# Performance work log

Hardware: AMD Instinct MI355X
Metric: run time of the kernel (lower is better)

## Reference

```python
import jax, jax.numpy as jnp
import numpy as np

N_NODES = 100000   # n_nodes
N_EDGES = 1600000  # n_nodes * avg_degree(16)
D_IN = 128
D_OUT = 128


def setup_inputs() -> dict:
    key = jax.random.key(0)
    k1, k2, k3, k4, k5 = jax.random.split(key, 5)
    h = jax.random.normal(k1, (N_NODES, D_IN), dtype=jnp.float32)
    edge_src = jax.random.randint(k2, (N_EDGES,), 0, N_NODES, dtype=jnp.int32)
    edge_dst = jax.random.randint(k3, (N_EDGES,), 0, N_NODES, dtype=jnp.int32)
    # Linear params, init per reset_parameters: U(-stdv, stdv), stdv = 1/sqrt(in_feats)
    stdv = 1.0 / np.sqrt(D_IN)
    W = jax.random.uniform(k4, (D_OUT, D_IN), dtype=jnp.float32, minval=-stdv, maxval=stdv)
    b = jax.random.uniform(k5, (D_OUT,), dtype=jnp.float32, minval=-stdv, maxval=stdv)
    return {"h": h, "edge_src": edge_src, "edge_dst": edge_dst, "W": W, "b": b}


def reference(h, edge_src, edge_dst, W, b):
    # update_all(copy_src('h'), sum) == neighbor-sum aggregation (SpMM with 0/1 adjacency)
    ah = jax.ops.segment_sum(h[edge_src], edge_dst, num_segments=N_NODES)  # [N, D_IN]
    # dense linear + activation fused on the aggregated features
    return jax.nn.relu(ah @ W.T + b)  # [N, D_OUT]
```

## Files before the change

### kernel.cpp

```cpp
#include <hip/hip_runtime.h>

#define D 128
#define BKT_SHIFT 9
#define BKT_SIZE 512
#define P1_EPB 4096
#define CNT_BLOCKS 512
#define PARTIALS_INTS (512 * 256)
#define SORT_CAP 9216
#define SW_LDU 68

typedef __attribute__((ext_vector_type(8))) short bf16x8;
typedef __attribute__((ext_vector_type(4))) float f32x4;

__device__ inline unsigned int pack2bf(float a, float b) {
    unsigned int ua = __float_as_uint(a);
    unsigned int ub = __float_as_uint(b);
    ua = (ua + 0x7fffu + ((ua >> 16) & 1u)) >> 16;
    ub = (ub + 0x7fffu + ((ub >> 16) & 1u)) >> 16;
    return ua | (ub << 16);
}
__device__ inline unsigned short pack1bf(float a) {
    unsigned int ua = __float_as_uint(a);
    return (unsigned short)((ua + 0x7fffu + ((ua >> 16) & 1u)) >> 16);
}


__global__ __launch_bounds__(256) void bucket_count_kernel(
    const int* __restrict__ edst, int* __restrict__ partials, int n_edges, int epb)
{
    __shared__ int hcnt[256];
    const int tid = threadIdx.x;
    hcnt[tid] = 0;
    __syncthreads();
    const int base = blockIdx.x * epb;
    const int lim = min(epb, n_edges - base);
    int k = tid;
    for (; k + 768 < lim; k += 1024) {
        int d0 = edst[base + k];
        int d1 = edst[base + k + 256];
        int d2 = edst[base + k + 512];
        int d3 = edst[base + k + 768];
        atomicAdd(&hcnt[d0 >> BKT_SHIFT], 1);
        atomicAdd(&hcnt[d1 >> BKT_SHIFT], 1);
        atomicAdd(&hcnt[d2 >> BKT_SHIFT], 1);
        atomicAdd(&hcnt[d3 >> BKT_SHIFT], 1);
    }
    for (; k < lim; k += 256)
        atomicAdd(&hcnt[edst[base + k] >> BKT_SHIFT], 1);
    __syncthreads();
    partials[(blockIdx.x << 8) + tid] = hcnt[tid];
}

__global__ __launch_bounds__(256) void bucket_scan_kernel(
    const int* __restrict__ partials, int* __restrict__ bucketBase,
    int* __restrict__ bucketCur, int nbk)
{
    __shared__ int s[256];
    const int t = threadIdx.x;
    int sum = 0;
    #pragma unroll 8
    for (int b = 0; b < CNT_BLOCKS; b++) sum += partials[(b << 8) + t];
    int v = (t < nbk) ? sum : 0;
    s[t] = v;
    __syncthreads();
    #pragma unroll
    for (int off = 1; off < 256; off <<= 1) {
        int x = (t >= off) ? s[t - off] : 0;
        __syncthreads();
        s[t] += x;
        __syncthreads();
    }
    if (t < nbk) {
        int base = s[t] - v;
        bucketBase[t] = base;
        bucketCur[t] = base;
    }
}

__global__ __launch_bounds__(256) void p1_partition_kernel(
    const int* __restrict__ esrc, const int* __restrict__ edst,
    int* __restrict__ bucketCur, unsigned int* __restrict__ pairs, int n_edges)
{
    __shared__ int hist[256];
    __shared__ int lbase[256];
    __shared__ int gbase[256];
    __shared__ int cur[256];
    __shared__ unsigned int buf[P1_EPB];
    __shared__ unsigned char bkt8[P1_EPB];
    const int tid = threadIdx.x;
    const int base = blockIdx.x * P1_EPB;
    hist[tid] = 0;
    __syncthreads();
    unsigned int pk[16]; int bk[16];
    #pragma unroll
    for (int k = 0; k < 16; k++) {
        int e = base + k * 256 + tid;
        if (e < n_edges) {
            int sv = esrc[e], dv = edst[e];
            bk[k] = dv >> BKT_SHIFT;
            pk[k] = ((unsigned)sv << BKT_SHIFT) | (unsigned)(dv & (BKT_SIZE - 1));
            atomicAdd(&hist[bk[k]], 1);
        } else bk[k] = -1;
    }
    __syncthreads();
    const int v = hist[tid];
    if (v > 0) gbase[tid] = atomicAdd(&bucketCur[tid], v);
    lbase[tid] = v;
    __syncthreads();
    #pragma unroll
    for (int off = 1; off < 256; off <<= 1) {
        int x = (tid >= off) ? lbase[tid - off] : 0;
        __syncthreads();
        lbase[tid] += x;
        __syncthreads();
    }
    const int excl = lbase[tid] - v;
    __syncthreads();
    lbase[tid] = excl;
    cur[tid] = excl;
    __syncthreads();
    #pragma unroll
    for (int k = 0; k < 16; k++) {
        if (bk[k] >= 0) {
            int loc = atomicAdd(&cur[bk[k]], 1);
            buf[loc] = pk[k];
            bkt8[loc] = (unsigned char)bk[k];
        }
    }
    __syncthreads();
    const int total = min(P1_EPB, n_edges - base);
    for (int i = tid; i < total; i += 256) {
        int b = bkt8[i];
        pairs[gbase[b] + (i - lbase[b])] = buf[i];
    }
}

__global__ __launch_bounds__(256) void p2_sort_gemm_kernel(
    const unsigned int* __restrict__ pairs, const int* __restrict__ bucketBase,
    int* __restrict__ sorted_src, int* __restrict__ gstart, int* __restrict__ gend,
    const float* __restrict__ h, const float* __restrict__ W,
    unsigned short* __restrict__ z,
    int n_nodes, int n_edges, int nbk)
{
    __shared__ union SU {
        struct { int hist[BKT_SIZE]; int cur[BKT_SIZE]; int sb[256]; int lbuf[SORT_CAP]; } s;
        unsigned int sW[128 * SW_LDU];
    } u;
    const int tid = threadIdx.x;

    if ((int)blockIdx.x < nbk) {
        const int bkt = blockIdx.x;
        const int nbase = bkt << BKT_SHIFT;
        const int pstart = bucketBase[bkt];
        const int pend = (bkt == nbk - 1) ? n_edges : bucketBase[bkt + 1];
        const int cnt = pend - pstart;
        u.s.hist[tid] = 0; u.s.hist[tid + 256] = 0;
        __syncthreads();
        {
            int j = pstart + tid;
            for (; j + 768 < pend; j += 1024) {
                unsigned int q0 = pairs[j];
                unsigned int q1 = pairs[j + 256];
                unsigned int q2 = pairs[j + 512];
                unsigned int q3 = pairs[j + 768];
                atomicAdd(&u.s.hist[q0 & (BKT_SIZE - 1)], 1);
                atomicAdd(&u.s.hist[q1 & (BKT_SIZE - 1)], 1);
                atomicAdd(&u.s.hist[q2 & (BKT_SIZE - 1)], 1);
                atomicAdd(&u.s.hist[q3 & (BKT_SIZE - 1)], 1);
            }
            for (; j < pend; j += 256)
                atomicAdd(&u.s.hist[pairs[j] & (BKT_SIZE - 1)], 1);
        }
        __syncthreads();
        int a  = u.s.hist[2 * tid];
        int b2 = u.s.hist[2 * tid + 1];
        int psum = a + b2;
        u.s.sb[tid] = psum;
        __syncthreads();
        #pragma unroll
        for (int off = 1; off < 256; off <<= 1) {
            int x = (tid >= off) ? u.s.sb[tid - off] : 0;
            __syncthreads();
            u.s.sb[tid] += x;
            __syncthreads();
        }
        int pexcl = u.s.sb[tid] - psum;
        u.s.cur[2 * tid] = pexcl;
        u.s.cur[2 * tid + 1] = pexcl + a;
        __syncthreads();
        for (int i = tid; i < BKT_SIZE; i += 256) {
            int nd = nbase + i;
            if (nd < n_nodes) {
                int st = pstart + u.s.cur[i];
                gstart[nd] = st;
                gend[nd] = st + u.s.hist[i];
            }
        }
        __syncthreads();
        if (cnt <= SORT_CAP) {
            {
                int j = pstart + tid;
                for (; j + 768 < pend; j += 1024) {
                    unsigned int q0 = pairs[j];
                    unsigned int q1 = pairs[j + 256];
                    unsigned int q2 = pairs[j + 512];
                    unsigned int q3 = pairs[j + 768];
                    int p0 = atomicAdd(&u.s.cur[q0 & (BKT_SIZE - 1)], 1);
                    int p1 = atomicAdd(&u.s.cur[q1 & (BKT_SIZE - 1)], 1);
                    int p2 = atomicAdd(&u.s.cur[q2 & (BKT_SIZE - 1)], 1);
                    int p3 = atomicAdd(&u.s.cur[q3 & (BKT_SIZE - 1)], 1);
                    u.s.lbuf[p0] = (int)(q0 >> BKT_SHIFT);
                    u.s.lbuf[p1] = (int)(q1 >> BKT_SHIFT);
                    u.s.lbuf[p2] = (int)(q2 >> BKT_SHIFT);
                    u.s.lbuf[p3] = (int)(q3 >> BKT_SHIFT);
                }
                for (; j < pend; j += 256) {
                    unsigned int p = pairs[j];
                    int pos = atomicAdd(&u.s.cur[p & (BKT_SIZE - 1)], 1);
                    u.s.lbuf[pos] = (int)(p >> BKT_SHIFT);
                }
            }
            __syncthreads();
            for (int i = tid; i < cnt; i += 256)
                sorted_src[pstart + i] = u.s.lbuf[i];
        } else {
            for (int j = pstart + tid; j < pend; j += 256) {
                unsigned int p = pairs[j];
                int local = p & (BKT_SIZE - 1);
                int pos = pstart + atomicAdd(&u.s.cur[local], 1);
                sorted_src[pos] = (int)(p >> BKT_SHIFT);
            }
        }
    } else {
        const int gbid = blockIdx.x - nbk;
        for (int i = tid; i < 4096; i += 256) {
            float4 w = ((const float4*)W)[i];
            int row = i >> 5, c4 = i & 31;
            unsigned int* dst = &u.sW[row * SW_LDU + c4 * 2];
            dst[0] = pack2bf(w.x, w.y);
            dst[1] = pack2bf(w.z, w.w);
        }
        __syncthreads();

        const int wave = tid >> 6;
        const int lane = tid & 63;
        const int m = lane & 15;
        const int q = lane >> 4;
        const int r0 = gbid * 64 + wave * 16;
        const int arow = r0 + m;
        const bool rvalid = arow < n_nodes;

        bf16x8 afrag[4];
        #pragma unroll
        for (int ks = 0; ks < 4; ks++) {
            float4 x = make_float4(0.f, 0.f, 0.f, 0.f), y = x;
            if (rvalid) {
                const float4* p = (const float4*)(h + (size_t)arow * D + ks * 32 + q * 8);
                x = p[0]; y = p[1];
            }
            union { unsigned int uu[4]; bf16x8 v; } cvt;
            cvt.uu[0] = pack2bf(x.x, x.y);
            cvt.uu[1] = pack2bf(x.z, x.w);
            cvt.uu[2] = pack2bf(y.x, y.y);
            cvt.uu[3] = pack2bf(y.z, y.w);
            afrag[ks] = cvt.v;
        }

        f32x4 acc[8];
        #pragma unroll
        for (int ct = 0; ct < 8; ct++) acc[ct] = (f32x4){0.f, 0.f, 0.f, 0.f};

        #pragma unroll
        for (int ct = 0; ct < 8; ct++) {
            #pragma unroll
            for (int ks = 0; ks < 4; ks++) {
                const unsigned int* p = &u.sW[(ct * 16 + m) * SW_LDU + ks * 16 + q * 4];
                union { uint4 uu; bf16x8 v; } bu;
                bu.uu = *(const uint4*)p;
                acc[ct] = __builtin_amdgcn_mfma_f32_16x16x32_bf16(afrag[ks], bu.v, acc[ct], 0, 0, 0);
            }
        }

        __syncthreads();
        unsigned short* lds_us = (unsigned short*)u.sW;
        #pragma unroll
        for (int ct = 0; ct < 8; ct++) {
            #pragma unroll
            for (int i = 0; i < 4; i++) {
                lds_us[(wave * 16 + q * 4 + i) * 130 + ct * 16 + m] = pack1bf(acc[ct][i]);
            }
        }
        __syncthreads();
        const unsigned int* lds32 = (const unsigned int*)u.sW;
        const int r0blk = gbid * 64;
        #pragma unroll
        for (int pass = 0; pass < 4; pass++) {
            int idx = pass * 256 + tid;
            int row = idx >> 4;
            int c16 = idx & 15;
            int r = r0blk + row;
            if (r < n_nodes) {
                int bo = row * 65 + c16 * 4;
                uint4 val;
                val.x = lds32[bo]; val.y = lds32[bo + 1];
                val.z = lds32[bo + 2]; val.w = lds32[bo + 3];
                ((uint4*)z)[(size_t)r * 16 + c16] = val;
            }
        }
    }
}

__global__ __launch_bounds__(256) void p2_sort_kernel(
    const unsigned int* __restrict__ pairs, const int* __restrict__ bucketBase,
    int* __restrict__ sorted_src, int* __restrict__ gstart, int* __restrict__ gend,
    int n_nodes, int n_edges, int nbk)
{
    __shared__ int hist[BKT_SIZE];
    __shared__ int cur[BKT_SIZE];
    __shared__ int sb[256];
    const int tid = threadIdx.x;
    const int bkt = blockIdx.x;
    const int nbase = bkt << BKT_SHIFT;
    const int pstart = bucketBase[bkt];
    const int pend = (bkt == nbk - 1) ? n_edges : bucketBase[bkt + 1];
    hist[tid] = 0; hist[tid + 256] = 0;
    __syncthreads();
    for (int j = pstart + tid; j < pend; j += 256)
        atomicAdd(&hist[pairs[j] & (BKT_SIZE - 1)], 1);
    __syncthreads();
    int a  = hist[2 * tid];
    int b2 = hist[2 * tid + 1];
    int psum = a + b2;
    sb[tid] = psum;
    __syncthreads();
    #pragma unroll
    for (int off = 1; off < 256; off <<= 1) {
        int x = (tid >= off) ? sb[tid - off] : 0;
        __syncthreads();
        sb[tid] += x;
        __syncthreads();
    }
    int pexcl = sb[tid] - psum;
    cur[2 * tid] = pexcl;
    cur[2 * tid + 1] = pexcl + a;
    __syncthreads();
    for (int i = tid; i < BKT_SIZE; i += 256) {
        int nd = nbase + i;
        if (nd < n_nodes) {
            int st = pstart + cur[i];
            gstart[nd] = st;
            gend[nd] = st + hist[i];
        }
    }
    __syncthreads();
    for (int j = pstart + tid; j < pend; j += 256) {
        unsigned int p = pairs[j];
        int local = p & (BKT_SIZE - 1);
        int pos = pstart + atomicAdd(&cur[local], 1);
        sorted_src[pos] = (int)(p >> BKT_SHIFT);
    }
}

__global__ __launch_bounds__(256) void gemm_z_kernel(
    const float* __restrict__ h, const float* __restrict__ W,
    unsigned short* __restrict__ z, int n_nodes)
{
    __shared__ unsigned int sW[128 * SW_LDU];
    const int tid = threadIdx.x;
    for (int i = tid; i < 4096; i += 256) {
        float4 w = ((const float4*)W)[i];
        int row = i >> 5, c4 = i & 31;
        unsigned int* dst = &sW[row * SW_LDU + c4 * 2];
        dst[0] = pack2bf(w.x, w.y);
        dst[1] = pack2bf(w.z, w.w);
    }
    __syncthreads();

    const int wave = tid >> 6;
    const int lane = tid & 63;
    const int m = lane & 15;
    const int q = lane >> 4;
    const int r0 = blockIdx.x * 64 + wave * 16;
    const int arow = r0 + m;
    const bool rvalid = arow < n_nodes;

    bf16x8 afrag[4];
    #pragma unroll
    for (int ks = 0; ks < 4; ks++) {
        float4 x = make_float4(0.f, 0.f, 0.f, 0.f), y = x;
        if (rvalid) {
            const float4* p = (const float4*)(h + (size_t)arow * D + ks * 32 + q * 8);
            x = p[0]; y = p[1];
        }
        union { unsigned int u[4]; bf16x8 v; } cvt;
        cvt.u[0] = pack2bf(x.x, x.y);
        cvt.u[1] = pack2bf(x.z, x.w);
        cvt.u[2] = pack2bf(y.x, y.y);
        cvt.u[3] = pack2bf(y.z, y.w);
        afrag[ks] = cvt.v;
    }

    f32x4 acc[8];
    #pragma unroll
    for (int ct = 0; ct < 8; ct++) acc[ct] = (f32x4){0.f, 0.f, 0.f, 0.f};

    #pragma unroll
    for (int ct = 0; ct < 8; ct++) {
        #pragma unroll
        for (int ks = 0; ks < 4; ks++) {
            const unsigned int* p = &sW[(ct * 16 + m) * SW_LDU + ks * 16 + q * 4];
            union { uint4 u; bf16x8 v; } bu;
            bu.u = *(const uint4*)p;
            acc[ct] = __builtin_amdgcn_mfma_f32_16x16x32_bf16(afrag[ks], bu.v, acc[ct], 0, 0, 0);
        }
    }

    __syncthreads();
    unsigned short* lds_us = (unsigned short*)sW;
    #pragma unroll
    for (int ct = 0; ct < 8; ct++) {
        #pragma unroll
        for (int i = 0; i < 4; i++) {
            lds_us[(wave * 16 + q * 4 + i) * 130 + ct * 16 + m] = pack1bf(acc[ct][i]);
        }
    }
    __syncthreads();
    const unsigned int* lds32 = (const unsigned int*)sW;
    const int r0blk = blockIdx.x * 64;
    #pragma unroll
    for (int pass = 0; pass < 4; pass++) {
        int idx = pass * 256 + tid;
        int row = idx >> 4;
        int c16 = idx & 15;
        int r = r0blk + row;
        if (r < n_nodes) {
            int bo = row * 65 + c16 * 4;
            uint4 val;
            val.x = lds32[bo]; val.y = lds32[bo + 1];
            val.z = lds32[bo + 2]; val.w = lds32[bo + 3];
            ((uint4*)z)[(size_t)r * 16 + c16] = val;
        }
    }
}

__global__ __launch_bounds__(256) void gather_row_kernel(
    const unsigned short* __restrict__ z, const int* __restrict__ gstart,
    const int* __restrict__ gend, const int* __restrict__ sorted_src,
    const float* __restrict__ b, float* __restrict__ out, int n_limit,
    int node_base)
{
    const int tid = threadIdx.x;
    const int node = node_base + blockIdx.x * 16 + (tid >> 4);
    const int lane = tid & 15;
    if (node >= n_limit) return;
    int e = gstart[node];
    const int end = gend[node];
    const uint4* __restrict__ z4 = (const uint4*)z;
    float acc[8];
    #pragma unroll
    for (int i = 0; i < 8; i++) acc[i] = 0.f;
#define ADDV(v) do { \
    acc[0] += __uint_as_float((v).x << 16); acc[1] += __uint_as_float((v).x & 0xffff0000u); \
    acc[2] += __uint_as_float((v).y << 16); acc[3] += __uint_as_float((v).y & 0xffff0000u); \
    acc[4] += __uint_as_float((v).z << 16); acc[5] += __uint_as_float((v).z & 0xffff0000u); \
    acc[6] += __uint_as_float((v).w << 16); acc[7] += __uint_as_float((v).w & 0xffff0000u); } while (0)
    for (; e + 4 <= end; e += 4) {
        int s0 = sorted_src[e + 0];
        int s1 = sorted_src[e + 1];
        int s2 = sorted_src[e + 2];
        int s3 = sorted_src[e + 3];
        uint4 v0 = z4[(size_t)s0 * 16 + lane];
        uint4 v1 = z4[(size_t)s1 * 16 + lane];
        uint4 v2 = z4[(size_t)s2 * 16 + lane];
        uint4 v3 = z4[(size_t)s3 * 16 + lane];
        ADDV(v0); ADDV(v1); ADDV(v2); ADDV(v3);
    }
    for (; e < end; e++) {
        uint4 v = z4[(size_t)sorted_src[e] * 16 + lane];
        ADDV(v);
    }
#undef ADDV
    float4 b0 = ((const float4*)b)[lane * 2];
    float4 b1 = ((const float4*)b)[lane * 2 + 1];
    float4* o = (float4*)(out + (size_t)node * D + lane * 8);
    o[0] = make_float4(fmaxf(acc[0] + b0.x, 0.f), fmaxf(acc[1] + b0.y, 0.f),
                       fmaxf(acc[2] + b0.z, 0.f), fmaxf(acc[3] + b0.w, 0.f));
    o[1] = make_float4(fmaxf(acc[4] + b1.x, 0.f), fmaxf(acc[5] + b1.y, 0.f),
                       fmaxf(acc[6] + b1.z, 0.f), fmaxf(acc[7] + b1.w, 0.f));
}


__global__ __launch_bounds__(256) void hist_kernel(
    const int* __restrict__ edst, int* __restrict__ cnt, int n_edges)
{
    int gid = blockIdx.x * 256 + threadIdx.x;
    if (gid < n_edges) atomicAdd(&cnt[edst[gid]], 1);
}

__global__ __launch_bounds__(256) void scanA_kernel(
    const int* __restrict__ cnt, int* __restrict__ localoff,
    int* __restrict__ blocksums, int n)
{
    __shared__ int s[256];
    const int t = threadIdx.x;
    const int base = blockIdx.x * 1024 + t * 4;
    int v[4]; int sum = 0;
    #pragma unroll
    for (int i = 0; i < 4; i++) {
        int idx = base + i;
        v[i] = (idx < n) ? cnt[idx] : 0;
        sum += v[i];
    }
    s[t] = sum;
    __syncthreads();
    #pragma unroll
    for (int off = 1; off < 256; off <<= 1) {
        int x = (t >= off) ? s[t - off] : 0;
        __syncthreads();
        s[t] += x;
        __syncthreads();
    }
    int excl = s[t] - sum;
    int run = 0;
    #pragma unroll
    for (int i = 0; i < 4; i++) {
        int idx = base + i;
        if (idx < n) localoff[idx] = excl + run;
        run += v[i];
    }
    if (t == 255) blocksums[blockIdx.x] = s[255];
}

__global__ __launch_bounds__(256) void scanB_kernel(
    const int* __restrict__ blocksums, int* __restrict__ blockoffs, int nb)
{
    __shared__ int s[256];
    const int t = threadIdx.x;
    int v = (t < nb) ? blocksums[t] : 0;
    s[t] = v;
    __syncthreads();
    #pragma unroll
    for (int off = 1; off < 256; off <<= 1) {
        int x = (t >= off) ? s[t - off] : 0;
        __syncthreads();
        s[t] += x;
        __syncthreads();
    }
    if (t < nb) blockoffs[t] = s[t] - v;
}

__global__ __launch_bounds__(256) void scanC_kernel(
    const int* __restrict__ localoff, const int* __restrict__ blockoffs,
    int* __restrict__ outoffs, int* __restrict__ cursor, int n)
{
    int gid = blockIdx.x * 256 + threadIdx.x;
    if (gid >= n) return;
    int v = localoff[gid] + blockoffs[blockIdx.x >> 2];
    outoffs[gid] = v;
    if (cursor) cursor[gid] = v;
}

__global__ __launch_bounds__(256) void place_kernel(
    const int* __restrict__ esrc, const int* __restrict__ edst,
    int* __restrict__ cursor, int* __restrict__ sorted_src, int n_edges)
{
    int gid = blockIdx.x * 256 + threadIdx.x;
    if (gid >= n_edges) return;
    int d = edst[gid];
    int pos = atomicAdd(&cursor[d], 1);
    sorted_src[pos] = esrc[gid];
}

__global__ __launch_bounds__(256) void gather_kernel(
    const float* __restrict__ h, const int* __restrict__ offs,
    const int* __restrict__ endp, const int* __restrict__ sorted_src,
    float* __restrict__ out, int n_nodes)
{
    const int tid = threadIdx.x;
    const int node = blockIdx.x * 8 + (tid >> 5);
    const int lane = tid & 31;
    if (node >= n_nodes) return;
    const int start = offs[node];
    const int end = endp[node];
    const float4* __restrict__ h4 = (const float4*)h;
    float4 acc = make_float4(0.f, 0.f, 0.f, 0.f);
    for (int e = start; e < end; e++) {
        float4 a = h4[(size_t)sorted_src[e] * 32 + lane];
        acc.x += a.x; acc.y += a.y; acc.z += a.z; acc.w += a.w;
    }
    ((float4*)out)[(size_t)node * 32 + lane] = acc;
}

__global__ __launch_bounds__(256) void scatter_kernel(
    const float* __restrict__ h, const int* __restrict__ esrc,
    const int* __restrict__ edst, float* __restrict__ out, int n_edges)
{
    int gid = blockIdx.x * 256 + threadIdx.x;
    int e = gid >> 5;
    int l = gid & 31;
    if (e >= n_edges) return;
    int s = esrc[e];
    int d = edst[e];
    float4 v = ((const float4*)(h + (size_t)s * D))[l];
    float* o = out + (size_t)d * D + (size_t)l * 4;
    atomicAdd(o + 0, v.x);
    atomicAdd(o + 1, v.y);
    atomicAdd(o + 2, v.z);
    atomicAdd(o + 3, v.w);
}

__global__ __launch_bounds__(256) void mfma_gemm_relu_kernel(
    float* __restrict__ io, const float* __restrict__ W,
    const float* __restrict__ b, int n_nodes)
{
    __shared__ unsigned int sW[128 * SW_LDU];
    const int tid = threadIdx.x;
    for (int i = tid; i < 4096; i += 256) {
        float4 w = ((const float4*)W)[i];
        int row = i >> 5, c4 = i & 31;
        unsigned int* dst = &sW[row * SW_LDU + c4 * 2];
        dst[0] = pack2bf(w.x, w.y);
        dst[1] = pack2bf(w.z, w.w);
    }
    __syncthreads();
    const int wave = tid >> 6;
    const int lane = tid & 63;
    const int m = lane & 15;
    const int q = lane >> 4;
    const int r0 = blockIdx.x * 64 + wave * 16;
    const int arow = r0 + m;
    const bool rvalid = arow < n_nodes;
    bf16x8 afrag[4];
    #pragma unroll
    for (int ks = 0; ks < 4; ks++) {
        float4 x = make_float4(0.f, 0.f, 0.f, 0.f), y = x;
        if (rvalid) {
            const float4* p = (const float4*)(io + (size_t)arow * D + ks * 32 + q * 8);
            x = p[0]; y = p[1];
        }
        union { unsigned int u[4]; bf16x8 v; } cvt;
        cvt.u[0] = pack2bf(x.x, x.y);
        cvt.u[1] = pack2bf(x.z, x.w);
        cvt.u[2] = pack2bf(y.x, y.y);
        cvt.u[3] = pack2bf(y.z, y.w);
        afrag[ks] = cvt.v;
    }
    f32x4 acc[8];
    #pragma unroll
    for (int ct = 0; ct < 8; ct++) acc[ct] = (f32x4){0.f, 0.f, 0.f, 0.f};
    #pragma unroll
    for (int ct = 0; ct < 8; ct++) {
        #pragma unroll
        for (int ks = 0; ks < 4; ks++) {
            const unsigned int* p = &sW[(ct * 16 + m) * SW_LDU + ks * 16 + q * 4];
            union { uint4 u; bf16x8 v; } bu;
            bu.u = *(const uint4*)p;
            acc[ct] = __builtin_amdgcn_mfma_f32_16x16x32_bf16(afrag[ks], bu.v, acc[ct], 0, 0, 0);
        }
    }
    #pragma unroll
    for (int ct = 0; ct < 8; ct++) {
        int col = ct * 16 + m;
        float bias = b[col];
        #pragma unroll
        for (int i = 0; i < 4; i++) {
            int r = r0 + q * 4 + i;
            if (r < n_nodes) {
                float v = acc[ct][i] + bias;
                io[(size_t)r * D + col] = v > 0.f ? v : 0.f;
            }
        }
    }
}

extern "C" void kernel_launch(void* const* d_in, const int* in_sizes, int n_in,
                              void* d_out, int out_size, void* d_ws, size_t ws_size,
                              hipStream_t stream) {
    const float* h    = (const float*)d_in[0];
    const int*   esrc = (const int*)d_in[1];
    const int*   edst = (const int*)d_in[2];
    const float* W    = (const float*)d_in[3];
    const float* b    = (const float*)d_in[4];
    float* out = (float*)d_out;
    const int n_nodes = in_sizes[0] / D;
    const int n_edges = in_sizes[1];
    const int NB  = (n_nodes + 1023) / 1024;
    const int NBK = (n_nodes + BKT_SIZE - 1) / BKT_SIZE;

    size_t fixed = ((size_t)2 * n_nodes + PARTIALS_INTS + 2 * NBK + (size_t)n_edges) * 4;
    size_t pairs_off = (fixed + 15) & ~(size_t)15;
    size_t z_off = (pairs_off + (size_t)n_edges * 4 + 15) & ~(size_t)15;
    size_t need_fused = z_off + (size_t)n_nodes * D * 2;

    size_t zone_bytes = (size_t)n_edges * 4;
    size_t zb2 = (size_t)n_nodes * D * 2;
    if (zb2 > zone_bytes) zone_bytes = zb2;
    size_t need_main = pairs_off + zone_bytes;

    const int cnt_epb = (n_edges + CNT_BLOCKS - 1) / CNT_BLOCKS;

    if (ws_size >= need_fused && NBK <= 256 && n_nodes <= (1 << 22)) {
        int* gstart     = (int*)d_ws;
        int* gend       = gstart + n_nodes;
        int* partials   = gend + n_nodes;
        int* bucketBase = partials + PARTIALS_INTS;
        int* bucketCur  = bucketBase + NBK;
        int* sorted_src = bucketCur + NBK;
        unsigned int* pairs = (unsigned int*)((char*)d_ws + pairs_off);
        unsigned short* z   = (unsigned short*)((char*)d_ws + z_off);

        bucket_count_kernel<<<CNT_BLOCKS, 256, 0, stream>>>(
            edst, partials, n_edges, cnt_epb);
        bucket_scan_kernel<<<1, 256, 0, stream>>>(partials, bucketBase, bucketCur, NBK);
        p1_partition_kernel<<<(n_edges + P1_EPB - 1) / P1_EPB, 256, 0, stream>>>(
            esrc, edst, bucketCur, pairs, n_edges);
        const int gemmBlocks = (n_nodes + 63) / 64;
        p2_sort_gemm_kernel<<<NBK + gemmBlocks, 256, 0, stream>>>(
            pairs, bucketBase, sorted_src, gstart, gend, h, W, z,
            n_nodes, n_edges, NBK);
        const int qa = (((n_nodes + 3) / 4) + 15) & ~15;
        int s = 0;
        while (s < n_nodes) {
            int e2 = min(s + qa, n_nodes);
            gather_row_kernel<<<(e2 - s + 15) / 16, 256, 0, stream>>>(
                z, gstart, gend, sorted_src, b, out, e2, s);
            s = e2;
        }
        return;
    }

    if (ws_size >= need_main && NBK <= 256 && n_nodes <= (1 << 23)) {
        int* gstart     = (int*)d_ws;
        int* gend       = gstart + n_nodes;
        int* partials   = gend + n_nodes;
        int* bucketBase = partials + PARTIALS_INTS;
        int* bucketCur  = bucketBase + NBK;
        int* sorted_src = bucketCur + NBK;
        void* zone = (char*)d_ws + pairs_off;
        unsigned int* pairs = (unsigned int*)zone;
        unsigned short* z = (unsigned short*)zone;

        bucket_count_kernel<<<CNT_BLOCKS, 256, 0, stream>>>(
            edst, partials, n_edges, cnt_epb);
        bucket_scan_kernel<<<1, 256, 0, stream>>>(partials, bucketBase, bucketCur, NBK);
        p1_partition_kernel<<<(n_edges + P1_EPB - 1) / P1_EPB, 256, 0, stream>>>(
            esrc, edst, bucketCur, pairs, n_edges);
        p2_sort_kernel<<<NBK, 256, 0, stream>>>(
            pairs, bucketBase, sorted_src, gstart, gend, n_nodes, n_edges, NBK);
        gemm_z_kernel<<<(n_nodes + 63) / 64, 256, 0, stream>>>(h, W, z, n_nodes);
        gather_row_kernel<<<(n_nodes + 15) / 16, 256, 0, stream>>>(
            z, gstart, gend, sorted_src, b, out, n_nodes, 0);
        return;
    }

    size_t csr_ints = (size_t)3 * n_nodes + 2 * NB + (size_t)n_edges;
    size_t needB = csr_ints * sizeof(int);
    if (ws_size >= needB && NB <= 256) {
        int* cnt        = (int*)d_ws;
        int* offs       = cnt + n_nodes;
        int* cursor     = offs + n_nodes;
        int* blocksums  = cursor + n_nodes;
        int* blockoffs  = blocksums + NB;
        int* sorted_src = blockoffs + NB;

        hipMemsetAsync(cnt, 0, (size_t)n_nodes * sizeof(int), stream);
        hist_kernel<<<(n_edges + 255) / 256, 256, 0, stream>>>(edst, cnt, n_edges);
        scanA_kernel<<<NB, 256, 0, stream>>>(cnt, offs, blocksums, n_nodes);
        scanB_kernel<<<1, 256, 0, stream>>>(blocksums, blockoffs, NB);
        scanC_kernel<<<(n_nodes + 255) / 256, 256, 0, stream>>>(
            offs, blockoffs, cnt, cursor, n_nodes);
        place_kernel<<<(n_edges + 255) / 256, 256, 0, stream>>>(
            esrc, edst, cursor, sorted_src, n_edges);
        gather_kernel<<<(n_nodes + 7) / 8, 256, 0, stream>>>(
            h, cnt, cursor, sorted_src, out, n_nodes);
    } else {
        hipMemsetAsync(out, 0, (size_t)n_nodes * D * sizeof(float), stream);
        long long total = (long long)n_edges * 32;
        scatter_kernel<<<(int)((total + 255) / 256), 256, 0, stream>>>(h, esrc, edst, out, n_edges);
    }
    mfma_gemm_relu_kernel<<<(n_nodes + 63) / 64, 256, 0, stream>>>(out, W, b, n_nodes);
}
```

Baseline: 258.5 us.

## Fuse bucket count, scan and partition into one cooperative kernel

Replaces the separate bucket count, single-block scan and partition launches with one cooperative kernel. It uses grid-wide syncs between phases and one block per 4096-edge chunk, so the count partials match the partition chunks. The gather stage, previously split into four launches, now runs as a single launch, and the unused fallback paths are removed. The aim is to cut launch gaps and inter-kernel drains. The cost is a serial scan on block 0 while every other block idles at the grid barrier.

Measured after the change: 371.6 us. 43.7% more time.

```diff
diff --git a/kernel.cpp b/kernel.cpp
--- a/kernel.cpp
+++ b/kernel.cpp
@@ -1,12 +1,14 @@
 #include <hip/hip_runtime.h>
+#include <hip/hip_cooperative_groups.h>
+
+namespace cg = cooperative_groups;
 
 #define D 128
 #define BKT_SHIFT 9
 #define BKT_SIZE 512
 #define P1_EPB 4096
-#define CNT_BLOCKS 512
-#define PARTIALS_INTS (512 * 256)
 #define SORT_CAP 9216
+#define COOP_MAX_BLOCKS 1536
 #define SW_LDU 68
 
 typedef __attribute__((ext_vector_type(8))) short bf16x8;
@@ -22,6 +24,116 @@
 __device__ inline unsigned short pack1bf(float a) {
     unsigned int ua = __float_as_uint(a);
     return (unsigned short)((ua + 0x7fffu + ((ua >> 16) & 1u)) >> 16);
+}
+
+__global__ __launch_bounds__(256) void build_coop_kernel(
+    const int* __restrict__ esrc, const int* __restrict__ edst,
+    int* __restrict__ partials, int* __restrict__ bucketBase,
+    int* __restrict__ bucketCur, unsigned int* __restrict__ pairs,
+    int n_edges, int nbk, int nchunks)
+{
+    cg::grid_group grid = cg::this_grid();
+    __shared__ int hist[256];
+    __shared__ int lbase[256];
+    __shared__ int gbase[256];
+    __shared__ int cur[256];
+    __shared__ unsigned int buf[P1_EPB];
+    __shared__ unsigned char bkt8[P1_EPB];
+    const int tid = threadIdx.x;
+
+    for (int c = blockIdx.x; c < nchunks; c += gridDim.x) {
+        hist[tid] = 0;
+        __syncthreads();
+        const int base = c * P1_EPB;
+        const int lim = min(P1_EPB, n_edges - base);
+        int k = tid;
+        for (; k + 768 < lim; k += 1024) {
+            int d0 = edst[base + k];
+            int d1 = edst[base + k + 256];
+            int d2 = edst[base + k + 512];
+            int d3 = edst[base + k + 768];
+            atomicAdd(&hist[d0 >> BKT_SHIFT], 1);
+            atomicAdd(&hist[d1 >> BKT_SHIFT], 1);
+            atomicAdd(&hist[d2 >> BKT_SHIFT], 1);
+            atomicAdd(&hist[d3 >> BKT_SHIFT], 1);
+        }
+        for (; k < lim; k += 256)
+            atomicAdd(&hist[edst[base + k] >> BKT_SHIFT], 1);
+        __syncthreads();
+        partials[(c << 8) + tid] = hist[tid];
+        __syncthreads();
+    }
+    grid.sync();
+
+    if (blockIdx.x == 0) {
+        int sum = 0;
+        for (int c2 = 0; c2 < nchunks; c2++) sum += partials[(c2 << 8) + tid];
+        int v = (tid < nbk) ? sum : 0;
+        lbase[tid] = v;
+        __syncthreads();
+        #pragma unroll
+        for (int off = 1; off < 256; off <<= 1) {
+            int x = (tid >= off) ? lbase[tid - off] : 0;
+            __syncthreads();
+            lbase[tid] += x;
+            __syncthreads();
+        }
+        if (tid < nbk) {
+            int b0 = lbase[tid] - v;
+            bucketBase[tid] = b0;
+            bucketCur[tid] = b0;
+        }
+    }
+    grid.sync();
+
+    for (int c = blockIdx.x; c < nchunks; c += gridDim.x) {
+        const int base = c * P1_EPB;
+        hist[tid] = 0;
+        __syncthreads();
+        unsigned int pk[16]; int bk[16];
+        #pragma unroll
+        for (int k = 0; k < 16; k++) {
+            int e = base + k * 256 + tid;
+            if (e < n_edges) {
+                int sv = esrc[e], dv = edst[e];
+                bk[k] = dv >> BKT_SHIFT;
+                pk[k] = ((unsigned)sv << BKT_SHIFT) | (unsigned)(dv & (BKT_SIZE - 1));
+                atomicAdd(&hist[bk[k]], 1);
+            } else bk[k] = -1;
+        }
+        __syncthreads();
+        const int v = hist[tid];
+        if (v > 0) gbase[tid] = atomicAdd(&bucketCur[tid], v);
+        lbase[tid] = v;
+        __syncthreads();
+        #pragma unroll
+        for (int off = 1; off < 256; off <<= 1) {
+            int x = (tid >= off) ? lbase[tid - off] : 0;
+            __syncthreads();
+            lbase[tid] += x;
+            __syncthreads();
+        }
+        const int excl = lbase[tid] - v;
+        __syncthreads();
+        lbase[tid] = excl;
+        cur[tid] = excl;
+        __syncthreads();
+        #pragma unroll
+        for (int k = 0; k < 16; k++) {
+            if (bk[k] >= 0) {
+                int loc = atomicAdd(&cur[bk[k]], 1);
+                buf[loc] = pk[k];
+                bkt8[loc] = (unsigned char)bk[k];
+            }
+        }
+        __syncthreads();
+        const int total = min(P1_EPB, n_edges - base);
+        for (int i = tid; i < total; i += 256) {
+            int b = bkt8[i];
+            pairs[gbase[b] + (i - lbase[b])] = buf[i];
+        }
+        __syncthreads();
+    }
 }
 
 
@@ -53,13 +165,12 @@
 
 __global__ __launch_bounds__(256) void bucket_scan_kernel(
     const int* __restrict__ partials, int* __restrict__ bucketBase,
-    int* __restrict__ bucketCur, int nbk)
+    int* __restrict__ bucketCur, int nbk, int nchunks)
 {
     __shared__ int s[256];
     const int t = threadIdx.x;
     int sum = 0;
-    #pragma unroll 8
-    for (int b = 0; b < CNT_BLOCKS; b++) sum += partials[(b << 8) + t];
+    for (int b = 0; b < nchunks; b++) sum += partials[(b << 8) + t];
     int v = (t < nbk) ? sum : 0;
     s[t] = v;
     __syncthreads();
@@ -310,139 +421,6 @@
     }
 }
 
-__global__ __launch_bounds__(256) void p2_sort_kernel(
-    const unsigned int* __restrict__ pairs, const int* __restrict__ bucketBase,
-    int* __restrict__ sorted_src, int* __restrict__ gstart, int* __restrict__ gend,
-    int n_nodes, int n_edges, int nbk)
-{
-    __shared__ int hist[BKT_SIZE];
-    __shared__ int cur[BKT_SIZE];
-    __shared__ int sb[256];
-    const int tid = threadIdx.x;
-    const int bkt = blockIdx.x;
-    const int nbase = bkt << BKT_SHIFT;
-    const int pstart = bucketBase[bkt];
-    const int pend = (bkt == nbk - 1) ? n_edges : bucketBase[bkt + 1];
-    hist[tid] = 0; hist[tid + 256] = 0;
-    __syncthreads();
-    for (int j = pstart + tid; j < pend; j += 256)
-        atomicAdd(&hist[pairs[j] & (BKT_SIZE - 1)], 1);
-    __syncthreads();
-    int a  = hist[2 * tid];
-    int b2 = hist[2 * tid + 1];
-    int psum = a + b2;
-    sb[tid] = psum;
-    __syncthreads();
-    #pragma unroll
-    for (int off = 1; off < 256; off <<= 1) {
-        int x = (tid >= off) ? sb[tid - off] : 0;
-        __syncthreads();
-        sb[tid] += x;
-        __syncthreads();
-    }
-    int pexcl = sb[tid] - psum;
-    cur[2 * tid] = pexcl;
-    cur[2 * tid + 1] = pexcl + a;
-    __syncthreads();
-    for (int i = tid; i < BKT_SIZE; i += 256) {
-        int nd = nbase + i;
-        if (nd < n_nodes) {
-            int st = pstart + cur[i];
-            gstart[nd] = st;
-            gend[nd] = st + hist[i];
-        }
-    }
-    __syncthreads();
-    for (int j = pstart + tid; j < pend; j += 256) {
-        unsigned int p = pairs[j];
-        int local = p & (BKT_SIZE - 1);
-        int pos = pstart + atomicAdd(&cur[local], 1);
-        sorted_src[pos] = (int)(p >> BKT_SHIFT);
-    }
-}
-
-__global__ __launch_bounds__(256) void gemm_z_kernel(
-    const float* __restrict__ h, const float* __restrict__ W,
-    unsigned short* __restrict__ z, int n_nodes)
-{
-    __shared__ unsigned int sW[128 * SW_LDU];
-    const int tid = threadIdx.x;
-    for (int i = tid; i < 4096; i += 256) {
-        float4 w = ((const float4*)W)[i];
-        int row = i >> 5, c4 = i & 31;
-        unsigned int* dst = &sW[row * SW_LDU + c4 * 2];
-        dst[0] = pack2bf(w.x, w.y);
-        dst[1] = pack2bf(w.z, w.w);
-    }
-    __syncthreads();
-
-    const int wave = tid >> 6;
-    const int lane = tid & 63;
-    const int m = lane & 15;
-    const int q = lane >> 4;
-    const int r0 = blockIdx.x * 64 + wave * 16;
-    const int arow = r0 + m;
-    const bool rvalid = arow < n_nodes;
-
-    bf16x8 afrag[4];
-    #pragma unroll
-    for (int ks = 0; ks < 4; ks++) {
-        float4 x = make_float4(0.f, 0.f, 0.f, 0.f), y = x;
-        if (rvalid) {
-            const float4* p = (const float4*)(h + (size_t)arow * D + ks * 32 + q * 8);
-            x = p[0]; y = p[1];
-        }
-        union { unsigned int u[4]; bf16x8 v; } cvt;
-        cvt.u[0] = pack2bf(x.x, x.y);
-        cvt.u[1] = pack2bf(x.z, x.w);
-        cvt.u[2] = pack2bf(y.x, y.y);
-        cvt.u[3] = pack2bf(y.z, y.w);
-        afrag[ks] = cvt.v;
-    }
-
-    f32x4 acc[8];
-    #pragma unroll
-    for (int ct = 0; ct < 8; ct++) acc[ct] = (f32x4){0.f, 0.f, 0.f, 0.f};
-
-    #pragma unroll
-    for (int ct = 0; ct < 8; ct++) {
-        #pragma unroll
-        for (int ks = 0; ks < 4; ks++) {
-            const unsigned int* p = &sW[(ct * 16 + m) * SW_LDU + ks * 16 + q * 4];
-            union { uint4 u; bf16x8 v; } bu;
-            bu.u = *(const uint4*)p;
-            acc[ct] = __builtin_amdgcn_mfma_f32_16x16x32_bf16(afrag[ks], bu.v, acc[ct], 0, 0, 0);
-        }
-    }
-
-    __syncthreads();
-    unsigned short* lds_us = (unsigned short*)sW;
-    #pragma unroll
-    for (int ct = 0; ct < 8; ct++) {
-        #pragma unroll
-        for (int i = 0; i < 4; i++) {
-            lds_us[(wave * 16 + q * 4 + i) * 130 + ct * 16 + m] = pack1bf(acc[ct][i]);
-        }
-    }
-    __syncthreads();
-    const unsigned int* lds32 = (const unsigned int*)sW;
-    const int r0blk = blockIdx.x * 64;
-    #pragma unroll
-    for (int pass = 0; pass < 4; pass++) {
-        int idx = pass * 256 + tid;
-        int row = idx >> 4;
-        int c16 = idx & 15;
-        int r = r0blk + row;
-        if (r < n_nodes) {
-            int bo = row * 65 + c16 * 4;
-            uint4 val;
-            val.x = lds32[bo]; val.y = lds32[bo + 1];
-            val.z = lds32[bo + 2]; val.w = lds32[bo + 3];
-            ((uint4*)z)[(size_t)r * 16 + c16] = val;
-        }
-    }
-}
-
 __global__ __launch_bounds__(256) void gather_row_kernel(
     const unsigned short* __restrict__ z, const int* __restrict__ gstart,
     const int* __restrict__ gend, const int* __restrict__ sorted_src,
@@ -490,107 +468,6 @@
 }
 
 
-__global__ __launch_bounds__(256) void hist_kernel(
-    const int* __restrict__ edst, int* __restrict__ cnt, int n_edges)
-{
-    int gid = blockIdx.x * 256 + threadIdx.x;
-    if (gid < n_edges) atomicAdd(&cnt[edst[gid]], 1);
-}
-
-__global__ __launch_bounds__(256) void scanA_kernel(
-    const int* __restrict__ cnt, int* __restrict__ localoff,
-    int* __restrict__ blocksums, int n)
-{
-    __shared__ int s[256];
-    const int t = threadIdx.x;
-    const int base = blockIdx.x * 1024 + t * 4;
-    int v[4]; int sum = 0;
-    #pragma unroll
-    for (int i = 0; i < 4; i++) {
-        int idx = base + i;
-        v[i] = (idx < n) ? cnt[idx] : 0;
-        sum += v[i];
-    }
-    s[t] = sum;
-    __syncthreads();
-    #pragma unroll
-    for (int off = 1; off < 256; off <<= 1) {
-        int x = (t >= off) ? s[t - off] : 0;
-        __syncthreads();
-        s[t] += x;
-        __syncthreads();
-    }
-    int excl = s[t] - sum;
-    int run = 0;
-    #pragma unroll
-    for (int i = 0; i < 4; i++) {
-        int idx = base + i;
-        if (idx < n) localoff[idx] = excl + run;
-        run += v[i];
-    }
-    if (t == 255) blocksums[blockIdx.x] = s[255];
-}
-
-__global__ __launch_bounds__(256) void scanB_kernel(
-    const int* __restrict__ blocksums, int* __restrict__ blockoffs, int nb)
-{
-    __shared__ int s[256];
-    const int t = threadIdx.x;
-    int v = (t < nb) ? blocksums[t] : 0;
-    s[t] = v;
-    __syncthreads();
-    #pragma unroll
-    for (int off = 1; off < 256; off <<= 1) {
-        int x = (t >= off) ? s[t - off] : 0;
-        __syncthreads();
-        s[t] += x;
-        __syncthreads();
-    }
-    if (t < nb) blockoffs[t] = s[t] - v;
-}
-
-__global__ __launch_bounds__(256) void scanC_kernel(
-    const int* __restrict__ localoff, const int* __restrict__ blockoffs,
-    int* __restrict__ outoffs, int* __restrict__ cursor, int n)
-{
-    int gid = blockIdx.x * 256 + threadIdx.x;
-    if (gid >= n) return;
-    int v = localoff[gid] + blockoffs[blockIdx.x >> 2];
-    outoffs[gid] = v;
-    if (cursor) cursor[gid] = v;
-}
-
-__global__ __launch_bounds__(256) void place_kernel(
-    const int* __restrict__ esrc, const int* __restrict__ edst,
-    int* __restrict__ cursor, int* __restrict__ sorted_src, int n_edges)
-{
-    int gid = blockIdx.x * 256 + threadIdx.x;
-    if (gid >= n_edges) return;
-    int d = edst[gid];
-    int pos = atomicAdd(&cursor[d], 1);
-    sorted_src[pos] = esrc[gid];
-}
-
-__global__ __launch_bounds__(256) void gather_kernel(
-    const float* __restrict__ h, const int* __restrict__ offs,
-    const int* __restrict__ endp, const int* __restrict__ sorted_src,
-    float* __restrict__ out, int n_nodes)
-{
-    const int tid = threadIdx.x;
-    const int node = blockIdx.x * 8 + (tid >> 5);
-    const int lane = tid & 31;
-    if (node >= n_nodes) return;
-    const int start = offs[node];
-    const int end = endp[node];
-    const float4* __restrict__ h4 = (const float4*)h;
-    float4 acc = make_float4(0.f, 0.f, 0.f, 0.f);
-    for (int e = start; e < end; e++) {
-        float4 a = h4[(size_t)sorted_src[e] * 32 + lane];
-        acc.x += a.x; acc.y += a.y; acc.z += a.z; acc.w += a.w;
-    }
-    ((float4*)out)[(size_t)node * 32 + lane] = acc;
-}
-
 __global__ __launch_bounds__(256) void scatter_kernel(
     const float* __restrict__ h, const int* __restrict__ esrc,
     const int* __restrict__ edst, float* __restrict__ out, int n_edges)
@@ -684,99 +561,51 @@
     float* out = (float*)d_out;
     const int n_nodes = in_sizes[0] / D;
     const int n_edges = in_sizes[1];
-    const int NB  = (n_nodes + 1023) / 1024;
     const int NBK = (n_nodes + BKT_SIZE - 1) / BKT_SIZE;
-
-    size_t fixed = ((size_t)2 * n_nodes + PARTIALS_INTS + 2 * NBK + (size_t)n_edges) * 4;
+    const int nchunks = (n_edges + P1_EPB - 1) / P1_EPB;
+
+    size_t fixed = ((size_t)2 * n_nodes + (size_t)nchunks * 256 + 2 * NBK
+                    + (size_t)n_edges) * 4;
     size_t pairs_off = (fixed + 15) & ~(size_t)15;
     size_t z_off = (pairs_off + (size_t)n_edges * 4 + 15) & ~(size_t)15;
     size_t need_fused = z_off + (size_t)n_nodes * D * 2;
-
-    size_t zone_bytes = (size_t)n_edges * 4;
-    size_t zb2 = (size_t)n_nodes * D * 2;
-    if (zb2 > zone_bytes) zone_bytes = zb2;
-    size_t need_main = pairs_off + zone_bytes;
-
-    const int cnt_epb = (n_edges + CNT_BLOCKS - 1) / CNT_BLOCKS;
 
     if (ws_size >= need_fused && NBK <= 256 && n_nodes <= (1 << 22)) {
         int* gstart     = (int*)d_ws;
         int* gend       = gstart + n_nodes;
         int* partials   = gend + n_nodes;
-        int* bucketBase = partials + PARTIALS_INTS;
+        int* bucketBase = partials + (size_t)nchunks * 256;
         int* bucketCur  = bucketBase + NBK;
         int* sorted_src = bucketCur + NBK;
         unsigned int* pairs = (unsigned int*)((char*)d_ws + pairs_off);
         unsigned short* z   = (unsigned short*)((char*)d_ws + z_off);
 
-        bucket_count_kernel<<<CNT_BLOCKS, 256, 0, stream>>>(
-            edst, partials, n_edges, cnt_epb);
-        bucket_scan_kernel<<<1, 256, 0, stream>>>(partials, bucketBase, bucketCur, NBK);
-        p1_partition_kernel<<<(n_edges + P1_EPB - 1) / P1_EPB, 256, 0, stream>>>(
-            esrc, edst, bucketCur, pairs, n_edges);
+        if (nchunks <= COOP_MAX_BLOCKS) {
+            int ne = n_edges, nb = NBK, nc = nchunks;
+            void* args[] = { (void*)&esrc, (void*)&edst, (void*)&partials,
+                             (void*)&bucketBase, (void*)&bucketCur, (void*)&pairs,
+                             (void*)&ne, (void*)&nb, (void*)&nc };
+            hipLaunchCooperativeKernel((void*)build_coop_kernel,
+                dim3(nchunks), dim3(256), args, 0, stream);
+        } else {
+            bucket_count_kernel<<<nchunks, 256, 0, stream>>>(
+                edst, partials, n_edges, P1_EPB);
+            bucket_scan_kernel<<<1, 256, 0, stream>>>(
+                partials, bucketBase, bucketCur, NBK, nchunks);
+            p1_partition_kernel<<<nchunks, 256, 0, stream>>>(
+                esrc, edst, bucketCur, pairs, n_edges);
+        }
         const int gemmBlocks = (n_nodes + 63) / 64;
         p2_sort_gemm_kernel<<<NBK + gemmBlocks, 256, 0, stream>>>(
             pairs, bucketBase, sorted_src, gstart, gend, h, W, z,
             n_nodes, n_edges, NBK);
-        const int qa = (((n_nodes + 3) / 4) + 15) & ~15;
-        int s = 0;
-        while (s < n_nodes) {
-            int e2 = min(s + qa, n_nodes);
-            gather_row_kernel<<<(e2 - s + 15) / 16, 256, 0, stream>>>(
-                z, gstart, gend, sorted_src, b, out, e2, s);
-            s = e2;
-        }
-        return;
-    }
-
-    if (ws_size >= need_main && NBK <= 256 && n_nodes <= (1 << 23)) {
-        int* gstart     = (int*)d_ws;
-        int* gend       = gstart + n_nodes;
-        int* partials   = gend + n_nodes;
-        int* bucketBase = partials + PARTIALS_INTS;
-        int* bucketCur  = bucketBase + NBK;
-        int* sorted_src = bucketCur + NBK;
-        void* zone = (char*)d_ws + pairs_off;
-        unsigned int* pairs = (unsigned int*)zone;
-        unsigned short* z = (unsigned short*)zone;
-
-        bucket_count_kernel<<<CNT_BLOCKS, 256, 0, stream>>>(
-            edst, partials, n_edges, cnt_epb);
-        bucket_scan_kernel<<<1, 256, 0, stream>>>(partials, bucketBase, bucketCur, NBK);
-        p1_partition_kernel<<<(n_edges + P1_EPB - 1) / P1_EPB, 256, 0, stream>>>(
-            esrc, edst, bucketCur, pairs, n_edges);
-        p2_sort_kernel<<<NBK, 256, 0, stream>>>(
-            pairs, bucketBase, sorted_src, gstart, gend, n_nodes, n_edges, NBK);
-        gemm_z_kernel<<<(n_nodes + 63) / 64, 256, 0, stream>>>(h, W, z, n_nodes);
         gather_row_kernel<<<(n_nodes + 15) / 16, 256, 0, stream>>>(
             z, gstart, gend, sorted_src, b, out, n_nodes, 0);
         return;
     }
 
-    size_t csr_ints = (size_t)3 * n_nodes + 2 * NB + (size_t)n_edges;
-    size_t needB = csr_ints * sizeof(int);
-    if (ws_size >= needB && NB <= 256) {
-        int* cnt        = (int*)d_ws;
-        int* offs       = cnt + n_nodes;
-        int* cursor     = offs + n_nodes;
-        int* blocksums  = cursor + n_nodes;
-        int* blockoffs  = blocksums + NB;
-        int* sorted_src = blockoffs + NB;
-
-        hipMemsetAsync(cnt, 0, (size_t)n_nodes * sizeof(int), stream);
-        hist_kernel<<<(n_edges + 255) / 256, 256, 0, stream>>>(edst, cnt, n_edges);
-        scanA_kernel<<<NB, 256, 0, stream>>>(cnt, offs, blocksums, n_nodes);
-        scanB_kernel<<<1, 256, 0, stream>>>(blocksums, blockoffs, NB);
-        scanC_kernel<<<(n_nodes + 255) / 256, 256, 0, stream>>>(
-            offs, blockoffs, cnt, cursor, n_nodes);
-        place_kernel<<<(n_edges + 255) / 256, 256, 0, stream>>>(
-            esrc, edst, cursor, sorted_src, n_edges);
-        gather_kernel<<<(n_nodes + 7) / 8, 256, 0, stream>>>(
-            h, cnt, cursor, sorted_src, out, n_nodes);
-    } else {
-        hipMemsetAsync(out, 0, (size_t)n_nodes * D * sizeof(float), stream);
-        long long total = (long long)n_edges * 32;
-        scatter_kernel<<<(int)((total + 255) / 256), 256, 0, stream>>>(h, esrc, edst, out, n_edges);
-    }
+    hipMemsetAsync(out, 0, (size_t)n_nodes * D * sizeof(float), stream);
+    long long total = (long long)n_edges * 32;
+    scatter_kernel<<<(int)((total + 255) / 256), 256, 0, stream>>>(h, esrc, edst, out, n_edges);
     mfma_gemm_relu_kernel<<<(n_nodes + 63) / 64, 256, 0, stream>>>(out, W, b, n_nodes);
 }
```
